# Kernel tuning notes

Hardware: AMD Instinct MI355X
Metric: run time of the kernel (lower is better)

Reference implementation:

```python
import jax, jax.numpy as jnp
import numpy as np

B_SZ, L, D_IN, D_MODEL, N_LAYERS, D_STATE, D_OUT = 32, 1024, 128, 256, 4, 64, 10
N2 = D_STATE // 2  # complex conjugate-pair modes


def setup_inputs() -> dict:
    key = jax.random.key(0)
    ks = jax.random.split(key, 12)
    H, N = D_MODEL, N2
    x = jax.random.normal(ks[0], (B_SZ, L, D_IN), jnp.float32)
    enc_w = jax.random.normal(ks[1], (D_IN, H), jnp.float32) / np.float32(np.sqrt(D_IN))
    enc_b = jnp.zeros((H,), jnp.float32)
    # S4D-diag params (diag-lin measure, real_type=exp): A = -exp(A_re_log) + i*A_im
    log_dt = jax.random.uniform(ks[2], (N_LAYERS, H), jnp.float32,
                                minval=np.float32(np.log(1e-3)), maxval=np.float32(np.log(1e-1)))
    A_re_log = jnp.full((N_LAYERS, H, N), np.float32(np.log(0.5)), jnp.float32)
    A_im = jnp.broadcast_to(np.float32(np.pi) * jnp.arange(N, dtype=jnp.float32),
                            (N_LAYERS, H, N)).copy()
    B_re = jnp.ones((N_LAYERS, H, N), jnp.float32)
    B_im = jnp.zeros((N_LAYERS, H, N), jnp.float32)
    C_re = jax.random.normal(ks[3], (N_LAYERS, H, N), jnp.float32) * np.float32(0.5 ** 0.5)
    C_im = jax.random.normal(ks[4], (N_LAYERS, H, N), jnp.float32) * np.float32(0.5 ** 0.5)
    D = jax.random.normal(ks[5], (N_LAYERS, H), jnp.float32)
    ln_w = jnp.ones((N_LAYERS, H), jnp.float32)
    ln_b = jnp.zeros((N_LAYERS, H), jnp.float32)
    out_w = jax.random.normal(ks[6], (N_LAYERS, H, 2 * H), jnp.float32) / np.float32(np.sqrt(H))
    out_b = jnp.zeros((N_LAYERS, 2 * H), jnp.float32)
    dec_w = jax.random.normal(ks[7], (H, D_OUT), jnp.float32) / np.float32(np.sqrt(H))
    dec_b = jnp.zeros((D_OUT,), jnp.float32)
    return dict(x=x, enc_w=enc_w, enc_b=enc_b, log_dt=log_dt, A_re_log=A_re_log, A_im=A_im,
                B_re=B_re, B_im=B_im, C_re=C_re, C_im=C_im, D=D, ln_w=ln_w, ln_b=ln_b,
                out_w=out_w, out_b=out_b, dec_w=dec_w, dec_b=dec_b)


def _layernorm(x, w, b):
    m = x.mean(-1, keepdims=True)
    v = ((x - m) ** 2).mean(-1, keepdims=True)
    return (x - m) * jax.lax.rsqrt(v + 1e-5) * w + b


def _s4_block(u, log_dt, A_re_log, A_im, B_re, B_im, C_re, C_im, Dp, out_w, out_b):
    # u: (B, L, H). Diagonal S4 (S4D) with ZOH discretization, FFT long-conv.
    H, N = A_re_log.shape
    Lq = u.shape[1]
    A = -jnp.exp(A_re_log) + 1j * A_im            # (H, N) complex, Re<0 stable
    dt = jnp.exp(log_dt)[:, None]                 # (H, 1)
    Bc = B_re + 1j * B_im
    Cc = C_re + 1j * C_im
    dtA = dt * A                                  # (H, N)
    dA = jnp.exp(dtA)
    dB = Bc * (dA - 1.0) / A                      # ZOH input matrix
    # Vandermonde kernel: K[h, l] = 2 * Re( sum_n C*dB * exp(dtA)^l )
    ell = jnp.arange(Lq, dtype=jnp.float32)
    P = jnp.exp(dtA[:, :, None] * ell)            # (H, N, L)
    K = 2.0 * jnp.einsum('hn,hnl->hl', Cc * dB, P).real  # (H, L) float32
    # causal conv via FFT at length 2L
    n_fft = 2 * Lq
    Kf = jnp.fft.rfft(K, n=n_fft, axis=-1)        # (H, L+1)
    Uf = jnp.fft.rfft(u, n=n_fft, axis=1)         # (B, L+1, H)
    y = jnp.fft.irfft(Uf * Kf.T[None], n=n_fft, axis=1)[:, :Lq]  # (B, L, H)
    y = y + u * Dp                                # skip connection D*u
    y = jax.nn.gelu(y)
    z = y @ out_w + out_b                         # position-wise output linear
    return z[..., :H] * jax.nn.sigmoid(z[..., H:])  # GLU


def reference(x, enc_w, enc_b, log_dt, A_re_log, A_im, B_re, B_im, C_re, C_im, D,
              ln_w, ln_b, out_w, out_b, dec_w, dec_b):
    h = x @ enc_w + enc_b                         # encoder: (B, L, d_model)
    for i in range(N_LAYERS):                     # postnorm residual stack
        z = _s4_block(h, log_dt[i], A_re_log[i], A_im[i], B_re[i], B_im[i],
                      C_re[i], C_im[i], D[i], out_w[i], out_b[i])
        h = z + h
        h = _layernorm(h, ln_w[i], ln_b[i])
    return h @ dec_w + dec_b                      # decoder: (B, L, d_output)
```

## Files before the change

### kernel.cpp

```cpp
#include <hip/hip_runtime.h>
#include <hip/hip_bf16.h>
#include <math.h>

#define B_SZ    32
#define LSEQ    1024
#define DIN     128
#define HDIM    256
#define NLAYERS 4
#define NSTATE  32
#define DOUT    10
#define M_ROWS  (B_SZ*LSEQ)
#define CH      64
#define NCH     (LSEQ/CH)
#define NBC     (B_SZ*NCH)

typedef __hip_bfloat16 bf16;
typedef __attribute__((ext_vector_type(8))) short bf16x8;
typedef __attribute__((ext_vector_type(4))) float f32x4;

__device__ __forceinline__ unsigned short f2bu(float x) {
    bf16 b = __float2bfloat16(x);
    return *(unsigned short*)&b;
}
__device__ __forceinline__ float bu2f(unsigned short u) {
    bf16 b = *(bf16*)&u;
    return __bfloat162float(b);
}

__device__ __forceinline__ float4 s4param(const float* __restrict__ log_dt,
                                          const float* __restrict__ A_re_log,
                                          const float* __restrict__ A_im,
                                          const float* __restrict__ B_re,
                                          const float* __restrict__ B_im,
                                          const float* __restrict__ C_re,
                                          const float* __restrict__ C_im,
                                          int layer, int h, int n) {
    int hn = layer * HDIM + h;
    int idx = hn * NSTATE + n;
    float dt   = expf(log_dt[hn]);
    float Are  = -expf(A_re_log[idx]);
    float Aim  = A_im[idx];
    float dtAre = dt * Are, dtAim = dt * Aim;
    float ea   = expf(dtAre);
    float dAre = ea * cosf(dtAim), dAim = ea * sinf(dtAim);
    float nre = dAre - 1.0f, nim = dAim;
    float inv = 1.0f / (Are * Are + Aim * Aim);
    float tre = (nre * Are + nim * Aim) * inv;
    float tim = (nim * Are - nre * Aim) * inv;
    float Brv = B_re[idx], Biv = B_im[idx];
    float dBre = Brv * tre - Biv * tim;
    float dBim = Brv * tim + Biv * tre;
    float Crv = C_re[idx], Civ = C_im[idx];
    float Wre = Crv * dBre - Civ * dBim;
    float Wim = Crv * dBim + Civ * dBre;
    return make_float4(dtAre, dtAim, Wre, Wim);
}

#define VMB_ (NLAYERS*HDIM*64*32/256)
#define TDB_ ((NLAYERS*HDIM*66+255)/256)
#define PAB_ (NLAYERS*NSTATE*HDIM/256)
#define WCB_ (NLAYERS*512*256/256)
__global__ void k_setup(const float* __restrict__ log_dt, const float* __restrict__ A_re_log,
                        const float* __restrict__ A_im, const float* __restrict__ B_re,
                        const float* __restrict__ B_im, const float* __restrict__ C_re,
                        const float* __restrict__ C_im, const float* __restrict__ out_w,
                        const float* __restrict__ enc_w, float* __restrict__ Td,
                        bf16* __restrict__ Vg, bf16* __restrict__ Mg,
                        float2* __restrict__ PA64, bf16* __restrict__ Wt,
                        bf16* __restrict__ Wet) {
    const float inv2pi = 0.15915494309189535f;
    const float twopi  = 6.283185307179586f;
    int bx = blockIdx.x;
    if (bx < VMB_) {
        int gid = bx * 256 + threadIdx.x;
        int jp = (gid & 31) * 2;
        int row = gid >> 5;
        int comp = row & 63, h = (row >> 6) & 255, layer = row >> 14;
        int n = comp >> 1, isIm = comp & 1;
        float4 q = s4param(log_dt, A_re_log, A_im, B_re, B_im, C_re, C_im, layer, h, n);
        unsigned int vpk = 0, mpk = 0;
#pragma unroll
        for (int e = 0; e < 2; ++e) {
            int j = jp + e;
            float dv = (float)(63 - j);
            float magv = __expf(dv * q.x);
            float pr = dv * q.y * inv2pi;
            float th = (pr - floorf(pr)) * twopi;
            float c = __cosf(th), s = __sinf(th);
            float vre = magv * (q.z * c - q.w * s);
            float vim = magv * (q.z * s + q.w * c);
            vpk |= (unsigned int)f2bu(isIm ? vim : vre) << (16 * e);
            float dm = (float)(j + 1);
            float magm = __expf(dm * q.x);
            float pr2 = dm * q.y * inv2pi;
            float th2 = (pr2 - floorf(pr2)) * twopi;
            float mv = isIm ? (-2.f * magm * __sinf(th2)) : (2.f * magm * __cosf(th2));
            mpk |= (unsigned int)f2bu(mv) << (16 * e);
        }
        {
            int mtv = comp >> 4, frv = comp & 15;
            int ksv = jp >> 5, qdv = (jp >> 3) & 3, ev = jp & 7;
            size_t voff = (size_t)(layer * 256 + h) * 4096
                        + ((size_t)((mtv * 2 + ksv) * 64) + qdv * 16 + frv) * 8 + ev;
            ((unsigned int*)Vg)[voff >> 1] = vpk;
        }
        ((unsigned int*)Mg)[(size_t)row * 32 + (jp >> 1)] = mpk;
    } else if (bx < VMB_ + TDB_) {
        int gid = (bx - VMB_) * 256 + threadIdx.x;
        int d = gid % 66;
        int lh = gid / 66;
        if (lh < NLAYERS * HDIM && d < 65) {
            int layer = lh >> 8, h = lh & 255;
            float fd = (float)d;
            float acc = 0.f;
            for (int n = 0; n < NSTATE; ++n) {
                float4 q = s4param(log_dt, A_re_log, A_im, B_re, B_im, C_re, C_im, layer, h, n);
                float mag = __expf(fd * q.x);
                float pr = fd * q.y * inv2pi;
                float th = (pr - floorf(pr)) * twopi;
                acc += mag * (q.z * __cosf(th) - q.w * __sinf(th));
            }
            Td[(size_t)lh * 66 + d] = 2.f * acc;
        }
    } else if (bx < VMB_ + TDB_ + PAB_) {
        int idx = (bx - VMB_ - TDB_) * 256 + threadIdx.x;
        int h = idx & 255, n = (idx >> 8) & 31, layer = idx >> 13;
        float4 q = s4param(log_dt, A_re_log, A_im, B_re, B_im, C_re, C_im, layer, h, n);
        float e64 = expf(64.0f * q.x);
        float ph  = 64.0f * q.y;
        PA64[idx] = make_float2(e64 * cosf(ph), e64 * sinf(ph));
    } else if (bx < VMB_ + TDB_ + PAB_ + WCB_) {
        int idx = (bx - VMB_ - TDB_ - PAB_) * 256 + threadIdx.x;
        int k = idx & 255;
        int n = (idx >> 8) & 511;
        int layer = idx >> 17;
        size_t off = (size_t)layer * (512 * 256)
                   + ((size_t)((n >> 4) * 8 + (k >> 5)) * 64 + (((k >> 3) & 3) * 16 + (n & 15))) * 8
                   + (k & 7);
        Wt[off] = __float2bfloat16(out_w[((size_t)(layer * 256 + k)) * 512 + n]);
    } else {
        int idx = (bx - VMB_ - TDB_ - PAB_ - WCB_) * 256 + threadIdx.x;
        int k = idx & 127, n = idx >> 7;
        Wet[idx] = __float2bfloat16(enc_w[(size_t)k * HDIM + n]);
    }
}

__global__ __launch_bounds__(256) void k_enc2(const float* __restrict__ X, const bf16* __restrict__ Wet,
                                              const float* __restrict__ bias, bf16* __restrict__ H,
                                              bf16* __restrict__ Ut) {
    __shared__ bf16 A_s[128 * 136];
    __shared__ bf16 B_s[64 * 136];
    int tid = threadIdx.x;
    int lane = tid & 63, wv = tid >> 6, quad = lane >> 4, fr = lane & 15;
    int m0 = blockIdx.x * 128, n0 = blockIdx.y * 64;
#pragma unroll
    for (int i = 0; i < 16; ++i) {
        int q = tid + i * 256, row = q >> 5, seg = q & 31;
        float4 v = *(const float4*)&X[(size_t)(m0 + row) * DIN + seg * 4];
        bf16* dst = &A_s[row * 136 + seg * 4];
        dst[0] = __float2bfloat16(v.x); dst[1] = __float2bfloat16(v.y);
        dst[2] = __float2bfloat16(v.z); dst[3] = __float2bfloat16(v.w);
    }
#pragma unroll
    for (int i = 0; i < 4; ++i) {
        int q = tid + i * 256, row = q >> 4, seg = q & 15;
        *(uint4*)&B_s[row * 136 + seg * 8] = *(const uint4*)&Wet[(size_t)(n0 + row) * DIN + seg * 8];
    }
    __syncthreads();
    f32x4 acc[2][4];
#pragma unroll
    for (int mt = 0; mt < 2; ++mt)
#pragma unroll
        for (int nt = 0; nt < 4; ++nt) acc[mt][nt] = (f32x4){0.f, 0.f, 0.f, 0.f};
#pragma unroll
    for (int ks = 0; ks < 4; ++ks) {
        bf16x8 a[2], b[4];
#pragma unroll
        for (int mt = 0; mt < 2; ++mt)
            a[mt] = *(const bf16x8*)&A_s[(wv * 32 + mt * 16 + fr) * 136 + ks * 32 + quad * 8];
#pragma unroll
        for (int nt = 0; nt < 4; ++nt)
            b[nt] = *(const bf16x8*)&B_s[(nt * 16 + fr) * 136 + ks * 32 + quad * 8];
#pragma unroll
        for (int mt = 0; mt < 2; ++mt)
#pragma unroll
            for (int nt = 0; nt < 4; ++nt)
                acc[mt][nt] = __builtin_amdgcn_mfma_f32_16x16x32_bf16(a[mt], b[nt], acc[mt][nt], 0, 0, 0);
    }
    __syncthreads();
#pragma unroll
    for (int mt = 0; mt < 2; ++mt)
#pragma unroll
        for (int nt = 0; nt < 4; ++nt) {
            int n = n0 + nt * 16 + fr;
            float bv = bias[n];
#pragma unroll
            for (int r = 0; r < 4; ++r) {
                int m = m0 + wv * 32 + mt * 16 + quad * 4 + r;
                float hv = acc[mt][nt][r] + bv;
                bf16 hb = __float2bfloat16(hv);
                H[(size_t)m * HDIM + n] = hb;
                B_s[(nt * 16 + fr) * 136 + (wv * 32 + mt * 16 + quad * 4 + r)] = hb;
            }
        }
    __syncthreads();
#pragma unroll
    for (int i = 0; i < 4; ++i) {
        int q = tid + i * 256, row = q >> 4, seg = q & 15;
        *(uint4*)&Ut[(size_t)(n0 + row) * M_ROWS + m0 + seg * 8] = *(uint4*)&B_s[row * 136 + seg * 8];
    }
}

__global__ __launch_bounds__(256) void k_conv(const bf16* __restrict__ Ut,
                                              const bf16* __restrict__ Vg,
                                              const bf16* __restrict__ Mg,
                                              const float* __restrict__ Tdl,
                                              const float2* __restrict__ PA,
                                              const float* __restrict__ Dw,
                                              bf16* __restrict__ Yt) {
    __shared__ bf16 A_s[64 * 136];
    __shared__ bf16 Eo_s[128 * 72];
    int h = blockIdx.x, bc0 = blockIdx.y * 128;
    int tid = threadIdx.x;
    int lane = tid & 63, wv = tid >> 6, quad = lane >> 4, fr = lane & 15;
    const float* Tdh = Tdl + (size_t)h * 66;
    const bf16* Uh = Ut + (size_t)h * M_ROWS + (size_t)bc0 * 64;
    bf16x8 va[2][4], ub[2][2];
#pragma unroll
    for (int ks = 0; ks < 2; ++ks) {
#pragma unroll
        for (int mt = 0; mt < 4; ++mt)
            va[ks][mt] = *(const bf16x8*)&Vg[(size_t)h * 4096 + ((size_t)((mt * 2 + ks) * 64) + lane) * 8];
#pragma unroll
        for (int nf = 0; nf < 2; ++nf)
            ub[ks][nf] = *(const bf16x8*)&Uh[(size_t)(wv * 32 + nf * 16 + fr) * 64 + ks * 32 + quad * 8];
    }
#pragma unroll
    for (int i = 0; i < 2; ++i) {
        int q = tid + i * 256, comp = q >> 3, seg = q & 7;
        uint4 v = *(const uint4*)&Mg[((size_t)h * 64 + comp) * 64 + seg * 8];
        const bf16* pv = (const bf16*)&v;
#pragma unroll
        for (int e = 0; e < 8; ++e) A_s[(seg * 8 + e) * 136 + 64 + comp] = pv[e];
    }
#pragma unroll
    for (int i = 0; i < 8; ++i) {
        int q = tid + i * 256;
        int l = q >> 5, jp = (q & 31) * 2;
        int d0 = l - jp, d1 = d0 - 1;
        unsigned int pk = (unsigned int)f2bu(d0 >= 0 ? Tdh[d0] : 0.f)
                        | ((unsigned int)f2bu(d1 >= 0 ? Tdh[d1] : 0.f) << 16);
        *(unsigned int*)&A_s[l * 136 + jp] = pk;
    }
    f32x4 eacc[4][2];
#pragma unroll
    for (int mt = 0; mt < 4; ++mt)
#pragma unroll
        for (int nf = 0; nf < 2; ++nf) eacc[mt][nf] = (f32x4){0.f, 0.f, 0.f, 0.f};
#pragma unroll
    for (int ks = 0; ks < 2; ++ks)
#pragma unroll
        for (int mt = 0; mt < 4; ++mt)
#pragma unroll
            for (int nf = 0; nf < 2; ++nf)
                eacc[mt][nf] = __builtin_amdgcn_mfma_f32_16x16x32_bf16(va[ks][mt], ub[ks][nf], eacc[mt][nf], 0, 0, 0);
#pragma unroll
    for (int mt = 0; mt < 4; ++mt)
#pragma unroll
        for (int nf = 0; nf < 2; ++nf) {
            int bc = wv * 32 + nf * 16 + fr;
#pragma unroll
            for (int r = 0; r < 4; r += 2) {
                int comp = mt * 16 + quad * 4 + r;
                *(unsigned int*)&Eo_s[bc * 72 + comp] =
                    (unsigned int)f2bu(eacc[mt][nf][r]) | ((unsigned int)f2bu(eacc[mt][nf][r + 1]) << 16);
            }
        }
    __syncthreads();
    {
        int bl = tid >> 5, n = tid & 31;
        float2 a = PA[n * HDIM + h];
        float cr = 0.f, ci = 0.f;
#pragma unroll
        for (int c = 0; c < NCH; ++c) {
            int bc = bl * NCH + c;
            unsigned int* slot = (unsigned int*)&Eo_s[bc * 72 + 2 * n];
            unsigned int ev = *slot;
            *slot = (unsigned int)f2bu(cr) | ((unsigned int)f2bu(ci) << 16);
            float er = bu2f((unsigned short)(ev & 0xffff));
            float ei = bu2f((unsigned short)(ev >> 16));
            float nr = fmaf(a.x, cr, fmaf(-a.y, ci, er));
            ci = fmaf(a.x, ci, fmaf(a.y, cr, ei));
            cr = nr;
        }
    }
    __syncthreads();
    uint2 uvp[4][2];
#pragma unroll
    for (int mt = 0; mt < 4; ++mt)
#pragma unroll
        for (int nf = 0; nf < 2; ++nf)
            uvp[mt][nf] = *(const uint2*)&Uh[(size_t)(wv * 32 + nf * 16 + fr) * 64 + mt * 16 + quad * 4];
    f32x4 acc[4][2];
#pragma unroll
    for (int mt = 0; mt < 4; ++mt)
#pragma unroll
        for (int nf = 0; nf < 2; ++nf) acc[mt][nf] = (f32x4){0.f, 0.f, 0.f, 0.f};

#define LDAB(AA, BB, KS) do { \
    _Pragma("unroll") \
    for (int mt = 0; mt < 4; ++mt) \
        AA[mt] = *(const bf16x8*)&A_s[(mt * 16 + fr) * 136 + (KS) * 32 + quad * 8]; \
    _Pragma("unroll") \
    for (int nf = 0; nf < 2; ++nf) \
        BB[nf] = ((KS) < 2) ? ub[(KS) & 1][nf] \
               : *(const bf16x8*)&Eo_s[(wv * 32 + nf * 16 + fr) * 72 + ((KS) & 1) * 32 + quad * 8]; \
    } while (0)
#define MFMAC(AA, BB) do { \
    _Pragma("unroll") \
    for (int mt = 0; mt < 4; ++mt) \
        _Pragma("unroll") \
        for (int nf = 0; nf < 2; ++nf) \
            acc[mt][nf] = __builtin_amdgcn_mfma_f32_16x16x32_bf16(AA[mt], BB[nf], acc[mt][nf], 0, 0, 0); \
    } while (0)

    {
        bf16x8 aA[4], bA[2], aB[4], bB[2];
        LDAB(aA, bA, 0);
        LDAB(aB, bB, 1);
        MFMAC(aA, bA);
        LDAB(aA, bA, 2);
        MFMAC(aB, bB);
        LDAB(aB, bB, 3);
        MFMAC(aA, bA);
        MFMAC(aB, bB);
    }
#undef LDAB
#undef MFMAC

    float Dv = Dw[h];
#pragma unroll
    for (int mt = 0; mt < 4; ++mt)
#pragma unroll
        for (int nf = 0; nf < 2; ++nf) {
            int bcl = wv * 32 + nf * 16 + fr;
            const bf16* up = (const bf16*)&uvp[mt][nf];
#pragma unroll
            for (int r = 0; r < 4; ++r) {
                int l = mt * 16 + quad * 4 + r;
                float u = __bfloat162float(up[r]);
                float v = fmaf(Dv, u, acc[mt][nf][r]);
                float z2 = 1.5957691216057308f * (v + 0.044715f * v * v * v);
                float sg = __builtin_amdgcn_rcpf(1.f + __expf(-z2));
                Eo_s[bcl * 72 + l] = __float2bfloat16(v * sg);
            }
        }
    __syncthreads();
#pragma unroll
    for (int i = 0; i < 4; ++i) {
        int q = tid + i * 256, row = q >> 3, c8 = q & 7;
        *(uint4*)&Yt[(size_t)h * M_ROWS + (size_t)(bc0 + row) * 64 + c8 * 8] =
            *(uint4*)&Eo_s[row * 72 + c8 * 8];
    }
}

__global__ __launch_bounds__(256) void k_gluln(const bf16* __restrict__ Yt,
                                               const bf16* __restrict__ Wt,
                                               const float* __restrict__ wb,
                                               bf16* __restrict__ Hb,
                                               const float* __restrict__ w,
                                               const float* __restrict__ bbias,
                                               bf16* __restrict__ Ut,
                                               const float* __restrict__ dw,
                                               const float* __restrict__ db,
                                               float* __restrict__ outp, int mode) {
    __shared__ __align__(16) bf16 A_s[32 * 264];
    __shared__ float red[2][8][32];
    __shared__ float stat[2][32];
    __shared__ float w_s[256], b_s[256];
    __shared__ float db_s[16];
    int tid = threadIdx.x;
    int lane = tid & 63, wv = tid >> 6;
    int quad = lane >> 4, fr = lane & 15;
    int m0 = blockIdx.x * 32;
    int rr = tid & 31, qd = tid >> 5;
    w_s[tid] = w[tid]; b_s[tid] = bbias[tid];
    if (mode == 1 && tid < DOUT) db_s[tid] = db[tid];
    float bias1[4], bias2[4];
#pragma unroll
    for (int nt = 0; nt < 4; ++nt) {
        bias1[nt] = wb[wv * 64 + nt * 16 + fr];
        bias2[nt] = wb[HDIM + wv * 64 + nt * 16 + fr];
    }
    int mg = tid & 7, hg = tid >> 3;
    uint2 rowv[8];
#pragma unroll
    for (int e = 0; e < 8; ++e)
        rowv[e] = *(const uint2*)&Yt[(size_t)(hg * 8 + e) * M_ROWS + m0 + mg * 4];
    uint4 hbv[4];
#pragma unroll
    for (int i = 0; i < 4; ++i)
        hbv[i] = *(const uint4*)&Hb[(size_t)(m0 + rr) * HDIM + qd * 32 + i * 8];
    {
#pragma unroll
        for (int j = 0; j < 4; ++j) {
            unsigned int pk[4];
#pragma unroll
            for (int k2 = 0; k2 < 4; ++k2) {
                unsigned int lo = ((const unsigned short*)&rowv[2 * k2])[j];
                unsigned int hi = ((const unsigned short*)&rowv[2 * k2 + 1])[j];
                pk[k2] = lo | (hi << 16);
            }
            *(uint4*)&A_s[(mg * 4 + j) * 264 + hg * 8] = *(uint4*)pk;
        }
    }
    f32x4 acc1[2][4], acc2[2][4];
#pragma unroll
    for (int mt = 0; mt < 2; ++mt)
#pragma unroll
        for (int nt = 0; nt < 4; ++nt) {
            acc1[mt][nt] = (f32x4){0.f, 0.f, 0.f, 0.f};
            acc2[mt][nt] = (f32x4){0.f, 0.f, 0.f, 0.f};
        }
    __syncthreads();

#define LOAD_B(d1, d2, KS) do { \
    _Pragma("unroll") \
    for (int nt = 0; nt < 4; ++nt) { \
        d1[nt] = *(const bf16x8*)&Wt[((size_t)((wv * 4 + nt) * 8 + (KS)) * 64 + lane) * 8]; \
        d2[nt] = *(const bf16x8*)&Wt[((size_t)((16 + wv * 4 + nt) * 8 + (KS)) * 64 + lane) * 8]; \
    } } while (0)

#define LOAD_A(da, KS) do { \
    _Pragma("unroll") \
    for (int mt = 0; mt < 2; ++mt) \
        da[mt] = *(const bf16x8*)&A_s[(mt * 16 + fr) * 264 + (KS) * 32 + quad * 8]; \
    } while (0)

#define MFMA8(da, bb1, bb2) do { \
    _Pragma("unroll") \
    for (int mt = 0; mt < 2; ++mt) \
        _Pragma("unroll") \
        for (int nt = 0; nt < 4; ++nt) { \
            acc1[mt][nt] = __builtin_amdgcn_mfma_f32_16x16x32_bf16(da[mt], bb1[nt], acc1[mt][nt], 0, 0, 0); \
            acc2[mt][nt] = __builtin_amdgcn_mfma_f32_16x16x32_bf16(da[mt], bb2[nt], acc2[mt][nt], 0, 0, 0); \
        } } while (0)

    {
        bf16x8 p1[4], p2[4], q1[4], q2[4], aP[2], aQ[2];
        LOAD_B(p1, p2, 0); LOAD_A(aP, 0);
#pragma unroll
        for (int kp = 0; kp < 4; ++kp) {
            LOAD_B(q1, q2, 2 * kp + 1); LOAD_A(aQ, 2 * kp + 1);
            MFMA8(aP, p1, p2);
            if (kp < 3) { LOAD_B(p1, p2, 2 * kp + 2); LOAD_A(aP, 2 * kp + 2); }
            MFMA8(aQ, q1, q2);
        }
    }
#undef LOAD_B
#undef LOAD_A
#undef MFMA8

    __syncthreads();
#pragma unroll
    for (int mt = 0; mt < 2; ++mt)
#pragma unroll
        for (int nt = 0; nt < 4; ++nt) {
            int n = wv * 64 + nt * 16 + fr;
#pragma unroll
            for (int r = 0; r < 4; ++r) {
                int m = mt * 16 + quad * 4 + r;
                float z1 = acc1[mt][nt][r] + bias1[nt];
                float z2 = acc2[mt][nt][r] + bias2[nt];
                float sg = __builtin_amdgcn_rcpf(1.0f + __expf(-z2));
                A_s[m * 264 + n] = __float2bfloat16(z1 * sg);
            }
        }
    __syncthreads();
    float rv[32];
    float sum = 0.f, sq = 0.f;
#pragma unroll
    for (int i4 = 0; i4 < 4; ++i4) {
        uint4 gv = *(uint4*)&A_s[rr * 264 + qd * 32 + i4 * 8];
        const bf16* gp = (const bf16*)&gv;
        const bf16* hp = (const bf16*)&hbv[i4];
#pragma unroll
        for (int e = 0; e < 8; ++e) {
            float v = __bfloat162float(gp[e]) + __bfloat162float(hp[e]);
            rv[i4 * 8 + e] = v; sum += v; sq += v * v;
        }
    }
    red[0][qd][rr] = sum; red[1][qd][rr] = sq;
    __syncthreads();
    if (tid < 32) {
        float s = 0.f, s2 = 0.f;
#pragma unroll
        for (int q = 0; q < 8; ++q) { s += red[0][q][tid]; s2 += red[1][q][tid]; }
        float mean = s * (1.f / HDIM);
        float var = s2 * (1.f / HDIM) - mean * mean;
        stat[0][tid] = mean; stat[1][tid] = rsqrtf(var + 1e-5f);
    }
    __syncthreads();
    float mean = stat[0][rr], rstd = stat[1][rr];
#pragma unroll
    for (int j = 0; j < 32; ++j)
        rv[j] = (rv[j] - mean) * rstd * w_s[qd * 32 + j] + b_s[qd * 32 + j];
    if (mode == 0) {
        bf16* Hw = Hb + (size_t)(m0 + rr) * HDIM + qd * 32;
#pragma unroll
        for (int j = 0; j < 32; j += 8) {
            unsigned int pk[4];
#pragma unroll
            for (int e = 0; e < 4; ++e)
                pk[e] = (unsigned int)f2bu(rv[j + 2 * e]) | ((unsigned int)f2bu(rv[j + 2 * e + 1]) << 16);
            *(uint4*)&Hw[j] = *(uint4*)pk;
        }
        bf16* Up = Ut + (size_t)(qd * 32) * M_ROWS + m0 + rr;
#pragma unroll
        for (int j = 0; j < 32; ++j)
            Up[(size_t)j * M_ROWS] = __float2bfloat16(rv[j]);
    } else {
        float* dwf = (float*)A_s;
        for (int e = tid; e < HDIM * DOUT; e += 256) dwf[e] = dw[e];
        __syncthreads();
        float part[DOUT];
#pragma unroll
        for (int o = 0; o < DOUT; ++o) part[o] = 0.f;
#pragma unroll
        for (int j = 0; j < 32; ++j) {
            float tv = rv[j];
            const float* dr = &dwf[(qd * 32 + j) * DOUT];
#pragma unroll
            for (int o = 0; o < DOUT; ++o) part[o] = fmaf(tv, dr[o], part[o]);
        }
#pragma unroll
        for (int oc = 0; oc < 5; ++oc) {
            red[0][qd][rr] = part[2 * oc];
            red[1][qd][rr] = part[2 * oc + 1];
            __syncthreads();
            if (tid < 64) {
                int rl = tid & 31, ph = tid >> 5;
                float s = 0.f;
#pragma unroll
                for (int q = 0; q < 8; ++q) s += red[ph][q][rl];
                int o = 2 * oc + ph;
                outp[(size_t)(m0 + rl) * DOUT + o] = s + db_s[o];
            }
            __syncthreads();
        }
    }
}

extern "C" void kernel_launch(void* const* d_in, const int* in_sizes, int n_in,
                              void* d_out, int out_size, void* d_ws, size_t ws_size,
                              hipStream_t stream) {
    const float* x        = (const float*)d_in[0];
    const float* enc_w    = (const float*)d_in[1];
    const float* enc_b    = (const float*)d_in[2];
    const float* log_dt   = (const float*)d_in[3];
    const float* A_re_log = (const float*)d_in[4];
    const float* A_im     = (const float*)d_in[5];
    const float* B_re     = (const float*)d_in[6];
    const float* B_im     = (const float*)d_in[7];
    const float* C_re     = (const float*)d_in[8];
    const float* C_im     = (const float*)d_in[9];
    const float* Dp       = (const float*)d_in[10];
    const float* ln_w     = (const float*)d_in[11];
    const float* ln_b     = (const float*)d_in[12];
    const float* out_w    = (const float*)d_in[13];
    const float* out_b    = (const float*)d_in[14];
    const float* dec_w    = (const float*)d_in[15];
    const float* dec_b    = (const float*)d_in[16];
    float* outp = (float*)d_out;

    float* w = (float*)d_ws;
    const size_t PWE = (size_t)NLAYERS * NSTATE * HDIM;
    const size_t MH  = (size_t)M_ROWS * HDIM;
    const size_t VME = (size_t)NLAYERS * HDIM * 64 * 64;
    float2* PA64 = (float2*)(w + 4 * PWE);
    float*  Td   = w + 6 * PWE;
    bf16*   Hbuf = (bf16*)(Td + (size_t)NLAYERS * HDIM * 66);
    bf16*   Ut   = Hbuf + MH;
    bf16*   Yt   = Ut + MH;
    bf16*   Wt   = Yt + MH;
    bf16*   Wet  = Wt + (size_t)NLAYERS * 512 * HDIM;
    bf16*   Vg   = Wet + (size_t)HDIM * DIN;
    bf16*   Mg   = Vg + VME;

    {
        int total = VMB_ + TDB_ + PAB_ + WCB_ + HDIM * DIN / 256;
        k_setup<<<total, 256, 0, stream>>>(log_dt, A_re_log, A_im, B_re, B_im, C_re, C_im,
                                           out_w, enc_w, Td, Vg, Mg, PA64, Wt, Wet);
    }

    dim3 ge(M_ROWS / 128, HDIM / 64);
    k_enc2<<<ge, 256, 0, stream>>>(x, Wet, enc_b, Hbuf, Ut);

    dim3 gconv(HDIM, NBC / 128);
    for (int layer = 0; layer < NLAYERS; ++layer) {
        const float2* pal = PA64 + (size_t)layer * NSTATE * HDIM;
        const float*  tdl = Td + (size_t)layer * HDIM * 66;
        const bf16*   vgl = Vg + (size_t)layer * HDIM * 64 * 64;
        const bf16*   mgl = Mg + (size_t)layer * HDIM * 64 * 64;
        k_conv<<<gconv, 256, 0, stream>>>(Ut, vgl, mgl, tdl, pal, Dp + layer * HDIM, Yt);
        k_gluln<<<M_ROWS / 32, 256, 0, stream>>>(Yt, Wt + (size_t)layer * 512 * HDIM,
                                                 out_b + layer * 2 * HDIM, Hbuf,
                                                 ln_w + layer * HDIM, ln_b + layer * HDIM,
                                                 Ut, dec_w, dec_b, outp,
                                                 layer == NLAYERS - 1 ? 1 : 0);
    }
}
```

Measured before the change: 320.8 us.

## Widen GLU-LayerNorm blocks to 64 rows with 8 waves sharing weight tiles

```diff
diff --git a/kernel.cpp b/kernel.cpp
--- a/kernel.cpp
+++ b/kernel.cpp
@@ -364,44 +364,40 @@
     }
 }
 
-__global__ __launch_bounds__(256) void k_gluln(const bf16* __restrict__ Yt,
-                                               const bf16* __restrict__ Wt,
-                                               const float* __restrict__ wb,
-                                               bf16* __restrict__ Hb,
-                                               const float* __restrict__ w,
-                                               const float* __restrict__ bbias,
-                                               bf16* __restrict__ Ut,
-                                               const float* __restrict__ dw,
-                                               const float* __restrict__ db,
-                                               float* __restrict__ outp, int mode) {
-    __shared__ __align__(16) bf16 A_s[32 * 264];
-    __shared__ float red[2][8][32];
-    __shared__ float stat[2][32];
+__global__ __launch_bounds__(512, 4) void k_gluln(const bf16* __restrict__ Yt,
+                                                  const bf16* __restrict__ Wt,
+                                                  const float* __restrict__ wb,
+                                                  bf16* __restrict__ Hb,
+                                                  const float* __restrict__ w,
+                                                  const float* __restrict__ bbias,
+                                                  bf16* __restrict__ Ut,
+                                                  const float* __restrict__ dw,
+                                                  const float* __restrict__ db,
+                                                  float* __restrict__ outp, int mode) {
+    __shared__ __align__(16) bf16 A_s[64 * 264];
+    __shared__ float red[2][8][64];
+    __shared__ float stat[2][64];
     __shared__ float w_s[256], b_s[256];
     __shared__ float db_s[16];
     int tid = threadIdx.x;
     int lane = tid & 63, wv = tid >> 6;
     int quad = lane >> 4, fr = lane & 15;
-    int m0 = blockIdx.x * 32;
-    int rr = tid & 31, qd = tid >> 5;
-    w_s[tid] = w[tid]; b_s[tid] = bbias[tid];
+    int m0 = blockIdx.x * 64;
+    int rr = tid & 63, qd = tid >> 6;
+    if (tid < 256) { w_s[tid] = w[tid]; b_s[tid] = bbias[tid]; }
     if (mode == 1 && tid < DOUT) db_s[tid] = db[tid];
-    float bias1[4], bias2[4];
-#pragma unroll
-    for (int nt = 0; nt < 4; ++nt) {
-        bias1[nt] = wb[wv * 64 + nt * 16 + fr];
-        bias2[nt] = wb[HDIM + wv * 64 + nt * 16 + fr];
-    }
-    int mg = tid & 7, hg = tid >> 3;
-    uint2 rowv[8];
-#pragma unroll
-    for (int e = 0; e < 8; ++e)
-        rowv[e] = *(const uint2*)&Yt[(size_t)(hg * 8 + e) * M_ROWS + m0 + mg * 4];
-    uint4 hbv[4];
-#pragma unroll
-    for (int i = 0; i < 4; ++i)
-        hbv[i] = *(const uint4*)&Hb[(size_t)(m0 + rr) * HDIM + qd * 32 + i * 8];
+    float bias1[2], bias2[2];
+#pragma unroll
+    for (int nt = 0; nt < 2; ++nt) {
+        bias1[nt] = wb[wv * 32 + nt * 16 + fr];
+        bias2[nt] = wb[HDIM + wv * 32 + nt * 16 + fr];
+    }
     {
+        int mg = tid & 15, hg = tid >> 4;
+        uint2 rowv[8];
+#pragma unroll
+        for (int e = 0; e < 8; ++e)
+            rowv[e] = *(const uint2*)&Yt[(size_t)(hg * 8 + e) * M_ROWS + m0 + mg * 4];
 #pragma unroll
         for (int j = 0; j < 4; ++j) {
             unsigned int pk[4];
@@ -414,11 +410,11 @@
             *(uint4*)&A_s[(mg * 4 + j) * 264 + hg * 8] = *(uint4*)pk;
         }
     }
-    f32x4 acc1[2][4], acc2[2][4];
-#pragma unroll
-    for (int mt = 0; mt < 2; ++mt)
-#pragma unroll
-        for (int nt = 0; nt < 4; ++nt) {
+    f32x4 acc1[4][2], acc2[4][2];
+#pragma unroll
+    for (int mt = 0; mt < 4; ++mt)
+#pragma unroll
+        for (int nt = 0; nt < 2; ++nt) {
             acc1[mt][nt] = (f32x4){0.f, 0.f, 0.f, 0.f};
             acc2[mt][nt] = (f32x4){0.f, 0.f, 0.f, 0.f};
         }
@@ -426,47 +422,44 @@
 
 #define LOAD_B(d1, d2, KS) do { \
     _Pragma("unroll") \
-    for (int nt = 0; nt < 4; ++nt) { \
-        d1[nt] = *(const bf16x8*)&Wt[((size_t)((wv * 4 + nt) * 8 + (KS)) * 64 + lane) * 8]; \
-        d2[nt] = *(const bf16x8*)&Wt[((size_t)((16 + wv * 4 + nt) * 8 + (KS)) * 64 + lane) * 8]; \
+    for (int nt = 0; nt < 2; ++nt) { \
+        d1[nt] = *(const bf16x8*)&Wt[((size_t)((wv * 2 + nt) * 8 + (KS)) * 64 + lane) * 8]; \
+        d2[nt] = *(const bf16x8*)&Wt[((size_t)((16 + wv * 2 + nt) * 8 + (KS)) * 64 + lane) * 8]; \
     } } while (0)
 
-#define LOAD_A(da, KS) do { \
+#define DO_MFMA(bb1, bb2, KS) do { \
+    bf16x8 afr[4]; \
     _Pragma("unroll") \
-    for (int mt = 0; mt < 2; ++mt) \
-        da[mt] = *(const bf16x8*)&A_s[(mt * 16 + fr) * 264 + (KS) * 32 + quad * 8]; \
-    } while (0)
-
-#define MFMA8(da, bb1, bb2) do { \
+    for (int mt = 0; mt < 4; ++mt) \
+        afr[mt] = *(const bf16x8*)&A_s[(mt * 16 + fr) * 264 + (KS) * 32 + quad * 8]; \
     _Pragma("unroll") \
-    for (int mt = 0; mt < 2; ++mt) \
+    for (int mt = 0; mt < 4; ++mt) \
         _Pragma("unroll") \
-        for (int nt = 0; nt < 4; ++nt) { \
-            acc1[mt][nt] = __builtin_amdgcn_mfma_f32_16x16x32_bf16(da[mt], bb1[nt], acc1[mt][nt], 0, 0, 0); \
-            acc2[mt][nt] = __builtin_amdgcn_mfma_f32_16x16x32_bf16(da[mt], bb2[nt], acc2[mt][nt], 0, 0, 0); \
+        for (int nt = 0; nt < 2; ++nt) { \
+            acc1[mt][nt] = __builtin_amdgcn_mfma_f32_16x16x32_bf16(afr[mt], bb1[nt], acc1[mt][nt], 0, 0, 0); \
+            acc2[mt][nt] = __builtin_amdgcn_mfma_f32_16x16x32_bf16(afr[mt], bb2[nt], acc2[mt][nt], 0, 0, 0); \
         } } while (0)
 
     {
-        bf16x8 p1[4], p2[4], q1[4], q2[4], aP[2], aQ[2];
-        LOAD_B(p1, p2, 0); LOAD_A(aP, 0);
+        bf16x8 p1[2], p2[2], q1[2], q2[2];
+        LOAD_B(p1, p2, 0);
 #pragma unroll
         for (int kp = 0; kp < 4; ++kp) {
-            LOAD_B(q1, q2, 2 * kp + 1); LOAD_A(aQ, 2 * kp + 1);
-            MFMA8(aP, p1, p2);
-            if (kp < 3) { LOAD_B(p1, p2, 2 * kp + 2); LOAD_A(aP, 2 * kp + 2); }
-            MFMA8(aQ, q1, q2);
+            LOAD_B(q1, q2, 2 * kp + 1);
+            DO_MFMA(p1, p2, 2 * kp);
+            if (kp < 3) LOAD_B(p1, p2, 2 * kp + 2);
+            DO_MFMA(q1, q2, 2 * kp + 1);
         }
     }
 #undef LOAD_B
-#undef LOAD_A
-#undef MFMA8
-
-    __syncthreads();
-#pragma unroll
-    for (int mt = 0; mt < 2; ++mt)
-#pragma unroll
-        for (int nt = 0; nt < 4; ++nt) {
-            int n = wv * 64 + nt * 16 + fr;
+#undef DO_MFMA
+
+    __syncthreads();
+#pragma unroll
+    for (int mt = 0; mt < 4; ++mt)
+#pragma unroll
+        for (int nt = 0; nt < 2; ++nt) {
+            int n = wv * 32 + nt * 16 + fr;
 #pragma unroll
             for (int r = 0; r < 4; ++r) {
                 int m = mt * 16 + quad * 4 + r;
@@ -477,13 +470,15 @@
             }
         }
     __syncthreads();
+    const bf16* Hr = Hb + (size_t)(m0 + rr) * HDIM + qd * 32;
     float rv[32];
     float sum = 0.f, sq = 0.f;
 #pragma unroll
     for (int i4 = 0; i4 < 4; ++i4) {
         uint4 gv = *(uint4*)&A_s[rr * 264 + qd * 32 + i4 * 8];
+        uint4 hv4 = *(const uint4*)&Hr[i4 * 8];
         const bf16* gp = (const bf16*)&gv;
-        const bf16* hp = (const bf16*)&hbv[i4];
+        const bf16* hp = (const bf16*)&hv4;
 #pragma unroll
         for (int e = 0; e < 8; ++e) {
             float v = __bfloat162float(gp[e]) + __bfloat162float(hp[e]);
@@ -492,7 +487,7 @@
     }
     red[0][qd][rr] = sum; red[1][qd][rr] = sq;
     __syncthreads();
-    if (tid < 32) {
+    if (tid < 64) {
         float s = 0.f, s2 = 0.f;
 #pragma unroll
         for (int q = 0; q < 8; ++q) { s += red[0][q][tid]; s2 += red[1][q][tid]; }
@@ -521,7 +516,7 @@
             Up[(size_t)j * M_ROWS] = __float2bfloat16(rv[j]);
     } else {
         float* dwf = (float*)A_s;
-        for (int e = tid; e < HDIM * DOUT; e += 256) dwf[e] = dw[e];
+        for (int e = tid; e < HDIM * DOUT; e += 512) dwf[e] = dw[e];
         __syncthreads();
         float part[DOUT];
 #pragma unroll
@@ -538,8 +533,8 @@
             red[0][qd][rr] = part[2 * oc];
             red[1][qd][rr] = part[2 * oc + 1];
             __syncthreads();
-            if (tid < 64) {
-                int rl = tid & 31, ph = tid >> 5;
+            if (tid < 128) {
+                int rl = tid & 63, ph = tid >> 6;
                 float s = 0.f;
 #pragma unroll
                 for (int q = 0; q < 8; ++q) s += red[ph][q][rl];
@@ -603,7 +598,7 @@
         const bf16*   vgl = Vg + (size_t)layer * HDIM * 64 * 64;
         const bf16*   mgl = Mg + (size_t)layer * HDIM * 64 * 64;
         k_conv<<<gconv, 256, 0, stream>>>(Ut, vgl, mgl, tdl, pal, Dp + layer * HDIM, Yt);
-        k_gluln<<<M_ROWS / 32, 256, 0, stream>>>(Yt, Wt + (size_t)layer * 512 * HDIM,
+        k_gluln<<<M_ROWS / 64, 512, 0, stream>>>(Yt, Wt + (size_t)layer * 512 * HDIM,
                                                  out_b + layer * 2 * HDIM, Hbuf,
                                                  ln_w + layer * HDIM, ln_b + layer * HDIM,
                                                  Ut, dec_w, dec_b, outp,
```

After: 297.0 us. -7.4%, faster.
